# Optimization experiments

Hardware: AMD Instinct MI355X
Metric: run time of the kernel (lower is better)

Reference implementation:

```python
import jax, jax.numpy as jnp
import numpy as np

N_NODES = 50000
N_EDGES = 800000
IN_C, HID_C, OUT_C = 128, 128, 64


def setup_inputs() -> dict:
    key = jax.random.key(0)
    ks = jax.random.split(key, 12)
    glorot = lambda k, shape: jax.random.normal(k, shape, dtype=jnp.float32) * (2.0 / (shape[0] + shape[-1])) ** 0.5
    return {
        "x": jax.random.normal(ks[0], (N_NODES, IN_C), dtype=jnp.float32),
        "edge_index": jax.random.randint(ks[1], (2, N_EDGES), 0, N_NODES, dtype=jnp.int64),
        "W_s1": glorot(ks[2], (IN_C, HID_C)), "b_s1": jnp.zeros((HID_C,), jnp.float32),
        "W_s2": glorot(ks[3], (HID_C, HID_C)), "b_s2": jnp.zeros((HID_C,), jnp.float32),
        "W_m1": glorot(ks[4], (IN_C, HID_C)), "b_m1": jnp.zeros((HID_C,), jnp.float32),
        "W_m21": glorot(ks[5], (IN_C, HID_C)), "b_m21": jnp.zeros((HID_C,), jnp.float32),
        "W_m22": glorot(ks[6], (HID_C, HID_C)), "b_m22": jnp.zeros((HID_C,), jnp.float32),
        "W_att": glorot(ks[7], (HID_C, 1)), "b_att": jnp.zeros((1,), jnp.float32),
        "W_fc": glorot(ks[8], (2 * HID_C, OUT_C)), "b_fc": jnp.zeros((OUT_C,), jnp.float32),
    }


def _gcn_conv(x, W, b, src, dst, n_nodes):
    """PyG GCNConv: add self-loops, symmetric deg^-1/2 norm, linear, scatter-add, bias."""
    xw = x @ W  # [N, H]
    loop = jnp.arange(n_nodes, dtype=src.dtype)
    s = jnp.concatenate([src, loop])
    d = jnp.concatenate([dst, loop])
    ones = jnp.ones(s.shape[0], dtype=x.dtype)
    deg = jax.ops.segment_sum(ones, d, num_segments=n_nodes)  # in-degree incl. self loop
    dinv = jnp.where(deg > 0, jax.lax.rsqrt(deg), 0.0)
    norm = dinv[s] * dinv[d]  # [E+N]
    msg = xw[s] * norm[:, None]
    return jax.ops.segment_sum(msg, d, num_segments=n_nodes) + b


def reference(x, edge_index, W_s1, b_s1, W_s2, b_s2, W_m1, b_m1, W_m21, b_m21,
              W_m22, b_m22, W_att, b_att, W_fc, b_fc):
    n = x.shape[0]
    src, dst = edge_index[0], edge_index[1]
    # structural branch: two GCN layers
    h_struct = jax.nn.relu(_gcn_conv(x, W_s1, b_s1, src, dst, n))
    h_struct = jax.nn.relu(_gcn_conv(h_struct, W_s2, b_s2, src, dst, n))
    # meta branches
    h1 = jax.nn.relu(_gcn_conv(x, W_m1, b_m1, src, dst, n))
    h2 = jax.nn.relu(_gcn_conv(x, W_m21, b_m21, src, dst, n))
    h2 = jax.nn.relu(_gcn_conv(h2, W_m22, b_m22, src, dst, n))
    # attention-weighted fusion over the 2 branches
    H = jnp.stack([h1, h2], axis=1)  # [N, 2, H]
    attn_scores = H @ W_att + b_att  # [N, 2, 1]
    attn_weights = jax.nn.softmax(attn_scores, axis=1)
    h_meta = jnp.sum(attn_weights * H, axis=1)  # [N, H]
    h_comb = jnp.concatenate([h_struct, h_meta], axis=1)  # [N, 2H]
    return h_comb @ W_fc + b_fc  # [N, OUT_C]
```

## Files before the change

### kernel.cpp

```cpp
#include <hip/hip_runtime.h>
#include <hip/hip_bf16.h>

#define N_NODES 50000
#define N_EDGES 800000
#define IN_C 128
#define HID_C 128
#define OUT_C 64

#define SCAN_BS 256
#define SCAN_NB ((N_NODES + SCAN_BS - 1) / SCAN_BS)

typedef __attribute__((ext_vector_type(8))) short bf16x8;
typedef __attribute__((ext_vector_type(4))) float f32x4;

__device__ __forceinline__ ushort f2bf(float f) {
    unsigned u = __float_as_uint(f);
    return (ushort)((u + 0x7fffu + ((u >> 16) & 1u)) >> 16);
}
__device__ __forceinline__ float bf2f(ushort u) {
    return __uint_as_float(((unsigned)u) << 16);
}

__global__ void degree_kernel(const int* __restrict__ dst, int E, int* __restrict__ hist) {
    int e = blockIdx.x * blockDim.x + threadIdx.x;
    if (e < E) atomicAdd(&hist[dst[e]], 1);
}

__global__ void dinv_kernel(const int* __restrict__ hist, float* __restrict__ dinv, int n) {
    int i = blockIdx.x * blockDim.x + threadIdx.x;
    if (i < n) dinv[i] = rsqrtf((float)(hist[i] + 1));
}

__global__ __launch_bounds__(SCAN_BS)
void scan1_kernel(const int* __restrict__ hist, int* __restrict__ bsum, int n) {
    __shared__ int s[SCAN_BS];
    int t = threadIdx.x;
    int i = blockIdx.x * SCAN_BS + t;
    int v = (i < n) ? hist[i] : 0;
    s[t] = v;
    __syncthreads();
#pragma unroll
    for (int off = SCAN_BS / 2; off > 0; off >>= 1) {
        if (t < off) s[t] += s[t + off];
        __syncthreads();
    }
    if (t == 0) bsum[blockIdx.x] = s[0];
}

__global__ __launch_bounds__(SCAN_BS)
void scan2_kernel(int* __restrict__ bsum, int* __restrict__ bpre, int nb,
                  int* __restrict__ row_ptr_last, int n) {
    __shared__ int s[SCAN_BS];
    int t = threadIdx.x;
    int v = (t < nb) ? bsum[t] : 0;
    s[t] = v;
    __syncthreads();
#pragma unroll
    for (int off = 1; off < SCAN_BS; off <<= 1) {
        int tmp = (t >= off) ? s[t - off] : 0;
        __syncthreads();
        s[t] += tmp;
        __syncthreads();
    }
    if (t < nb) bpre[t] = s[t] - v;
    if (t == SCAN_BS - 1) row_ptr_last[n] = s[t];
}

__global__ __launch_bounds__(SCAN_BS)
void scan3_kernel(const int* __restrict__ hist, const int* __restrict__ bpre,
                  int* __restrict__ row_ptr, int* __restrict__ cursor, int n) {
    __shared__ int s[SCAN_BS];
    int t = threadIdx.x;
    int i = blockIdx.x * SCAN_BS + t;
    int v = (i < n) ? hist[i] : 0;
    s[t] = v;
    __syncthreads();
#pragma unroll
    for (int off = 1; off < SCAN_BS; off <<= 1) {
        int tmp = (t >= off) ? s[t - off] : 0;
        __syncthreads();
        s[t] += tmp;
        __syncthreads();
    }
    if (i < n) {
        int ex = s[t] - v + bpre[blockIdx.x];
        row_ptr[i] = ex;
        cursor[i]  = ex;
    }
}

__global__ void fill_kernel(const int* __restrict__ src, const int* __restrict__ dst, int E,
                            int* __restrict__ cursor, int2* __restrict__ edge_data,
                            const float* __restrict__ dinv) {
    int e = blockIdx.x * blockDim.x + threadIdx.x;
    if (e < E) {
        int d = dst[e];
        int s = src[e];
        int pos = atomicAdd(&cursor[d], 1);
        edge_data[pos] = make_int2(s, __float_as_int(dinv[s]));
    }
}

__global__ void cvt_bf16_kernel(const float* __restrict__ in, uint2* __restrict__ out, int n4) {
    int i = blockIdx.x * blockDim.x + threadIdx.x;
    if (i >= n4) return;
    float4 v = *(const float4*)&in[(size_t)i * 4];
    uint2 o;
    o.x = (uint)f2bf(v.x) | ((uint)f2bf(v.y) << 16);
    o.y = (uint)f2bf(v.z) | ((uint)f2bf(v.w) << 16);
    out[i] = o;
}

__global__ void pack_wcat_kernel(const float* __restrict__ Ws1, const float* __restrict__ Wm21,
                                 const float* __restrict__ Wm1,
                                 const float* __restrict__ bs1, const float* __restrict__ bm21,
                                 const float* __restrict__ bm1,
                                 ushort* __restrict__ Wt, float* __restrict__ bcat) {
    int idx = blockIdx.x * blockDim.x + threadIdx.x;
    if (idx < 384 * 128) {
        int c = idx >> 7, k = idx & 127;
        float v = (c < 128) ? Ws1[k * 128 + c]
                : (c < 256) ? Wm21[k * 128 + (c - 128)]
                            : Wm1[k * 128 + (c - 256)];
        Wt[idx] = f2bf(v);
    }
    if (idx < 384) {
        bcat[idx] = (idx < 128) ? bs1[idx] : (idx < 256) ? bm21[idx - 128] : bm1[idx - 256];
    }
}

__global__ void tpack_kernel(const float* __restrict__ W, ushort* __restrict__ Wt, int K, int C) {
    int idx = blockIdx.x * blockDim.x + threadIdx.x;
    if (idx >= K * C) return;
    int c = idx / K, k = idx % K;
    Wt[idx] = f2bf(W[(size_t)k * C + c]);
}

template<int C>
__global__ __launch_bounds__(256)
void agg_bf16(const ushort* __restrict__ X, int ldx,
              ushort* __restrict__ Y, int ldy,
              const int* __restrict__ row_ptr,
              const int2* __restrict__ edge_data,
              const float* __restrict__ dinv, int n) {
    constexpr int CG = C / 8;
    constexpr int SLOTS = 64 / CG;
    const int wid = blockIdx.x * (blockDim.x >> 6) + (threadIdx.x >> 6);
    if (wid >= n) return;
    const int lane = threadIdx.x & 63;
    const int cg = lane & (CG - 1);
    const int slot = lane / CG;

    const float di = dinv[wid];
    float acc[8] = {0.f, 0.f, 0.f, 0.f, 0.f, 0.f, 0.f, 0.f};

    auto fma_row = [&](uint4 v, float w) {
        acc[0] = fmaf(w, __uint_as_float(v.x << 16), acc[0]);
        acc[1] = fmaf(w, __uint_as_float(v.x & 0xffff0000u), acc[1]);
        acc[2] = fmaf(w, __uint_as_float(v.y << 16), acc[2]);
        acc[3] = fmaf(w, __uint_as_float(v.y & 0xffff0000u), acc[3]);
        acc[4] = fmaf(w, __uint_as_float(v.z << 16), acc[4]);
        acc[5] = fmaf(w, __uint_as_float(v.z & 0xffff0000u), acc[5]);
        acc[6] = fmaf(w, __uint_as_float(v.w << 16), acc[6]);
        acc[7] = fmaf(w, __uint_as_float(v.w & 0xffff0000u), acc[7]);
    };

    if (slot == 0) {
        uint4 v = *(const uint4*)&X[(size_t)wid * ldx + cg * 8];
        fma_row(v, di * di);
    }
    const int e0 = row_ptr[wid], e1 = row_ptr[wid + 1];
    int e = e0 + slot;
    for (; e + SLOTS < e1; e += 2 * SLOTS) {
        const int2 d0 = edge_data[e];
        const int2 d1 = edge_data[e + SLOTS];
        const uint4 v0 = *(const uint4*)&X[(size_t)d0.x * ldx + cg * 8];
        const uint4 v1 = *(const uint4*)&X[(size_t)d1.x * ldx + cg * 8];
        fma_row(v0, di * __int_as_float(d0.y));
        fma_row(v1, di * __int_as_float(d1.y));
    }
    if (e < e1) {
        const int2 d0 = edge_data[e];
        const uint4 v0 = *(const uint4*)&X[(size_t)d0.x * ldx + cg * 8];
        fma_row(v0, di * __int_as_float(d0.y));
    }
#pragma unroll
    for (int j = 0; j < 8; ++j) {
        if (SLOTS == 4) acc[j] += __shfl_xor(acc[j], 16);
        if (SLOTS >= 2) acc[j] += __shfl_xor(acc[j], 32);
    }
    if (slot == 0) {
        uint4 o;
        o.x = (uint)f2bf(acc[0]) | ((uint)f2bf(acc[1]) << 16);
        o.y = (uint)f2bf(acc[2]) | ((uint)f2bf(acc[3]) << 16);
        o.z = (uint)f2bf(acc[4]) | ((uint)f2bf(acc[5]) << 16);
        o.w = (uint)f2bf(acc[6]) | ((uint)f2bf(acc[7]) << 16);
        *(uint4*)&Y[(size_t)wid * ldy + cg * 8] = o;
    }
}

__global__ __launch_bounds__(256)
void mfma_gemm_kernel(const ushort* __restrict__ A, int lda,
                      const ushort* __restrict__ Wt,
                      const float* __restrict__ bias,
                      void* __restrict__ Yv, int ldy,
                      int M, int relu, int obf16) {
    __shared__ char Asmem[128 * 272];
    const int tid = threadIdx.x;
    const int lane = tid & 63;
    const int w = tid >> 6;
    const int rb = blockIdx.x * 128;
    const int cb = blockIdx.y * 128;

    {
        const int rowbase = tid >> 4;
        const int inrow = (tid & 15) * 8;
#pragma unroll
        for (int it = 0; it < 8; ++it) {
            int row = it * 16 + rowbase;
            uint4 v = make_uint4(0u, 0u, 0u, 0u);
            int r = rb + row;
            if (r < M) v = *(const uint4*)&A[(size_t)r * lda + inrow];
            *(uint4*)&Asmem[row * 272 + (tid & 15) * 16] = v;
        }
    }
    __syncthreads();

    f32x4 acc[2][8];
#pragma unroll
    for (int i = 0; i < 2; ++i)
#pragma unroll
        for (int j = 0; j < 8; ++j) acc[i][j] = (f32x4){0.f, 0.f, 0.f, 0.f};

    const int arow0 = w * 32 + (lane & 15);
    const int kq = (lane >> 4) * 8;
    const int ccol = lane & 15;
#pragma unroll
    for (int ks = 0; ks < 4; ++ks) {
        const int k0 = ks * 32;
        const bf16x8 a0 = *(const bf16x8*)&Asmem[arow0 * 272 + (k0 + kq) * 2];
        const bf16x8 a1 = *(const bf16x8*)&Asmem[(arow0 + 16) * 272 + (k0 + kq) * 2];
#pragma unroll
        for (int ct = 0; ct < 8; ++ct) {
            const bf16x8 b = *(const bf16x8*)&Wt[(size_t)(cb + ct * 16 + ccol) * 128 + k0 + kq];
            acc[0][ct] = __builtin_amdgcn_mfma_f32_16x16x32_bf16(a0, b, acc[0][ct], 0, 0, 0);
            acc[1][ct] = __builtin_amdgcn_mfma_f32_16x16x32_bf16(a1, b, acc[1][ct], 0, 0, 0);
        }
    }

    const int rowq = (lane >> 4) * 4;
#pragma unroll
    for (int rt = 0; rt < 2; ++rt) {
#pragma unroll
        for (int ct = 0; ct < 8; ++ct) {
            const int col = cb + ct * 16 + ccol;
            const float bcol = bias[col];
#pragma unroll
            for (int r = 0; r < 4; ++r) {
                const int row = rb + w * 32 + rt * 16 + rowq + r;
                if (row >= M) continue;
                float v = acc[rt][ct][r] + bcol;
                if (relu) v = fmaxf(v, 0.f);
                if (obf16) ((ushort*)Yv)[(size_t)row * ldy + col] = f2bf(v);
                else       ((float*)Yv)[(size_t)row * ldy + col] = v;
            }
        }
    }
}

__global__ __launch_bounds__(256)
void gemm_kernel(const float* __restrict__ X, int ldx,
                 const float* __restrict__ W, int ldw,
                 const float* __restrict__ bias,
                 void* __restrict__ Yv, int ldy,
                 int nrows, int K, int relu, int obf16) {
    __shared__ float Xs[64][68];
    __shared__ float Ws[64][68];
    const int tid = threadIdx.x;
    const int tx = tid & 15;
    const int ty = tid >> 4;
    const int rb = blockIdx.x * 64;
    const int cb = blockIdx.y * 64;

    float acc[4][4] = {{0.f}};

    for (int k0 = 0; k0 < K; k0 += 64) {
#pragma unroll
        for (int q = 0; q < 4; ++q) {
            int idx = tid + q * 256;
            int row = idx >> 4;
            int kq  = idx & 15;
            float4 v = make_float4(0.f, 0.f, 0.f, 0.f);
            int r = rb + row;
            if (r < nrows) v = *(const float4*)&X[(size_t)r * ldx + k0 + kq * 4];
            Xs[kq * 4 + 0][row] = v.x;
            Xs[kq * 4 + 1][row] = v.y;
            Xs[kq * 4 + 2][row] = v.z;
            Xs[kq * 4 + 3][row] = v.w;
        }
#pragma unroll
        for (int q = 0; q < 4; ++q) {
            int idx = tid + q * 256;
            int k  = idx >> 4;
            int c4 = idx & 15;
            float4 v = *(const float4*)&W[(size_t)(k0 + k) * ldw + cb + c4 * 4];
            *(float4*)&Ws[k][c4 * 4] = v;
        }
        __syncthreads();
#pragma unroll 16
        for (int k = 0; k < 64; ++k) {
            const float4 xv = *(const float4*)&Xs[k][ty * 4];
            const float4 wv = *(const float4*)&Ws[k][tx * 4];
            const float xr[4] = {xv.x, xv.y, xv.z, xv.w};
            const float wr[4] = {wv.x, wv.y, wv.z, wv.w};
#pragma unroll
            for (int i = 0; i < 4; ++i)
#pragma unroll
                for (int j = 0; j < 4; ++j)
                    acc[i][j] = fmaf(xr[i], wr[j], acc[i][j]);
        }
        __syncthreads();
    }

    const float4 bv = *(const float4*)&bias[cb + tx * 4];
    const float br[4] = {bv.x, bv.y, bv.z, bv.w};
#pragma unroll
    for (int i = 0; i < 4; ++i) {
        int r = rb + ty * 4 + i;
        if (r >= nrows) continue;
        float v0 = acc[i][0] + br[0];
        float v1 = acc[i][1] + br[1];
        float v2 = acc[i][2] + br[2];
        float v3 = acc[i][3] + br[3];
        if (relu) {
            v0 = fmaxf(v0, 0.f); v1 = fmaxf(v1, 0.f);
            v2 = fmaxf(v2, 0.f); v3 = fmaxf(v3, 0.f);
        }
        if (obf16) {
            ushort4 o;
            o.x = f2bf(v0); o.y = f2bf(v1); o.z = f2bf(v2); o.w = f2bf(v3);
            *(ushort4*)&((ushort*)Yv)[(size_t)r * ldy + cb + tx * 4] = o;
        } else {
            *(float4*)&((float*)Yv)[(size_t)r * ldy + cb + tx * 4] = make_float4(v0, v1, v2, v3);
        }
    }
}

__global__ __launch_bounds__(64)
void attn_kernel(const ushort* __restrict__ h1bf, const float* __restrict__ h2,
                 const float* __restrict__ Watt, const float* __restrict__ batt,
                 float* __restrict__ out, int ldout) {
    int i = blockIdx.x;
    int l = threadIdx.x;
    const ushort* h1p = &h1bf[(size_t)i * 384 + 256];
    float w0 = Watt[l], w1w = Watt[l + 64];
    float h1a = bf2f(h1p[l]),               h1b = bf2f(h1p[l + 64]);
    float h2a = h2[(size_t)i * 128 + l],    h2b = h2[(size_t)i * 128 + l + 64];
    float a = h1a * w0 + h1b * w1w;
    float b = h2a * w0 + h2b * w1w;
#pragma unroll
    for (int off = 32; off > 0; off >>= 1) {
        a += __shfl_xor(a, off);
        b += __shfl_xor(b, off);
    }
    float ba = batt[0];
    a += ba; b += ba;
    float m  = fmaxf(a, b);
    float ea = __expf(a - m), eb = __expf(b - m);
    float inv = 1.f / (ea + eb);
    float wa = ea * inv, wb = eb * inv;
    out[(size_t)i * ldout + l]      = wa * h1a + wb * h2a;
    out[(size_t)i * ldout + l + 64] = wa * h1b + wb * h2b;
}

extern "C" void kernel_launch(void* const* d_in, const int* in_sizes, int n_in,
                              void* d_out, int out_size, void* d_ws, size_t ws_size,
                              hipStream_t stream) {
    const int N = N_NODES, E = N_EDGES;
    const float* x     = (const float*)d_in[0];
    const int*   ei    = (const int*)d_in[1];
    const int*   esrc  = ei;
    const int*   edst  = ei + E;
    const float* W_s1  = (const float*)d_in[2];
    const float* b_s1  = (const float*)d_in[3];
    const float* W_s2  = (const float*)d_in[4];
    const float* b_s2  = (const float*)d_in[5];
    const float* W_m1  = (const float*)d_in[6];
    const float* b_m1  = (const float*)d_in[7];
    const float* W_m21 = (const float*)d_in[8];
    const float* b_m21 = (const float*)d_in[9];
    const float* W_m22 = (const float*)d_in[10];
    const float* b_m22 = (const float*)d_in[11];
    const float* W_att = (const float*)d_in[12];
    const float* b_att = (const float*)d_in[13];
    const float* W_fc  = (const float*)d_in[14];
    const float* b_fc  = (const float*)d_in[15];
    float* out = (float*)d_out;

    char* base = (char*)d_ws;
    size_t off = 0;
    auto take = [&](size_t nbytes) -> void* {
        void* p = base + off;
        off += (nbytes + 255) & ~(size_t)255;
        return p;
    };
    int*    hist      = (int*)take((size_t)N * 4);
    int*    cursor    = (int*)take((size_t)N * 4);
    int*    row_ptr   = (int*)take((size_t)(N + 1) * 4);
    int*    bsum      = (int*)take((size_t)SCAN_NB * 4);
    int*    bpre      = (int*)take((size_t)SCAN_NB * 4);
    int2*   edge_data = (int2*)take((size_t)E * 8);
    float*  dinv      = (float*)take((size_t)N * 4);
    ushort* xb        = (ushort*)take((size_t)N * 128 * 2);
    ushort* agg_x     = (ushort*)take((size_t)N * 128 * 2);
    ushort* cat1      = (ushort*)take((size_t)N * 384 * 2);
    ushort* bufB      = (ushort*)take((size_t)N * 256 * 2);
    float*  comb      = (float*)take((size_t)N * 256 * 4);
    float*  h2buf     = (float*)take((size_t)N * 128 * 4);
    ushort* Wcat_t    = (ushort*)take((size_t)384 * 128 * 2);
    ushort* Ws2_t     = (ushort*)take((size_t)128 * 128 * 2);
    ushort* Wm22_t    = (ushort*)take((size_t)128 * 128 * 2);
    float*  bcat      = (float*)take((size_t)384 * 4);

    hipMemsetAsync(hist, 0, (size_t)N * 4, stream);
    degree_kernel<<<(E + 255) / 256, 256, 0, stream>>>(edst, E, hist);
    dinv_kernel<<<(N + 255) / 256, 256, 0, stream>>>(hist, dinv, N);
    scan1_kernel<<<SCAN_NB, SCAN_BS, 0, stream>>>(hist, bsum, N);
    scan2_kernel<<<1, SCAN_BS, 0, stream>>>(bsum, bpre, SCAN_NB, row_ptr, N);
    scan3_kernel<<<SCAN_NB, SCAN_BS, 0, stream>>>(hist, bpre, row_ptr, cursor, N);
    fill_kernel<<<(E + 255) / 256, 256, 0, stream>>>(esrc, edst, E, cursor, edge_data, dinv);

    cvt_bf16_kernel<<<(N * 128 / 4 + 255) / 256, 256, 0, stream>>>(x, (uint2*)xb, N * 128 / 4);
    pack_wcat_kernel<<<(384 * 128 + 255) / 256, 256, 0, stream>>>(W_s1, W_m21, W_m1,
                                                                  b_s1, b_m21, b_m1, Wcat_t, bcat);
    tpack_kernel<<<(128 * 128 + 255) / 256, 256, 0, stream>>>(W_s2, Ws2_t, 128, 128);
    tpack_kernel<<<(128 * 128 + 255) / 256, 256, 0, stream>>>(W_m22, Wm22_t, 128, 128);

    agg_bf16<128><<<(N + 3) / 4, 256, 0, stream>>>(xb, 128, agg_x, 128, row_ptr, edge_data, dinv, N);

    dim3 gm384((N + 127) / 128, 3);
    dim3 gm128((N + 127) / 128, 1);
    mfma_gemm_kernel<<<gm384, 256, 0, stream>>>(agg_x, 128, Wcat_t, bcat, cat1, 384, N, 1, 1);

    agg_bf16<256><<<(N + 3) / 4, 256, 0, stream>>>(cat1, 384, bufB, 256, row_ptr, edge_data, dinv, N);

    mfma_gemm_kernel<<<gm128, 256, 0, stream>>>(bufB, 256, Ws2_t, b_s2, comb, 256, N, 1, 0);
    mfma_gemm_kernel<<<gm128, 256, 0, stream>>>(bufB + 128, 256, Wm22_t, b_m22, h2buf, 128, N, 1, 0);

    attn_kernel<<<N, 64, 0, stream>>>(cat1, h2buf, W_att, b_att, comb + 128, 256);

    dim3 g64((N + 63) / 64, 1);
    gemm_kernel<<<g64, 256, 0, stream>>>(comb, 256, W_fc, 64, b_fc, out, 64, N, 256, 0, 0);
}
```

Before: 423.7 us.

## Replace FP32 final FC GEMM with bf16 MFMA kernel and store intermediates as bf16

The scalar FP32 tiled GEMM for the final fully connected layer is replaced with a bf16 MFMA kernel that stages a 64-row A tile in shared memory and reads transposed bf16 weights. The struct and meta-branch GEMM outputs and the attention output are now stored as bf16 rather than fp32, which halves their memory traffic. The aggregation loop is also unrolled to four edges per slot so more gathers are in flight. The cost is extra bf16 rounding on intermediate activations and one more weight-transpose launch.

After: 414.0 us. -2.3%, faster.

```diff
diff --git a/kernel.cpp b/kernel.cpp
--- a/kernel.cpp
+++ b/kernel.cpp
@@ -171,15 +171,21 @@
     }
     const int e0 = row_ptr[wid], e1 = row_ptr[wid + 1];
     int e = e0 + slot;
-    for (; e + SLOTS < e1; e += 2 * SLOTS) {
+    for (; e + 3 * SLOTS < e1; e += 4 * SLOTS) {
         const int2 d0 = edge_data[e];
         const int2 d1 = edge_data[e + SLOTS];
+        const int2 d2 = edge_data[e + 2 * SLOTS];
+        const int2 d3 = edge_data[e + 3 * SLOTS];
         const uint4 v0 = *(const uint4*)&X[(size_t)d0.x * ldx + cg * 8];
         const uint4 v1 = *(const uint4*)&X[(size_t)d1.x * ldx + cg * 8];
+        const uint4 v2 = *(const uint4*)&X[(size_t)d2.x * ldx + cg * 8];
+        const uint4 v3 = *(const uint4*)&X[(size_t)d3.x * ldx + cg * 8];
         fma_row(v0, di * __int_as_float(d0.y));
         fma_row(v1, di * __int_as_float(d1.y));
-    }
-    if (e < e1) {
+        fma_row(v2, di * __int_as_float(d2.y));
+        fma_row(v3, di * __int_as_float(d3.y));
+    }
+    for (; e < e1; e += SLOTS) {
         const int2 d0 = edge_data[e];
         const uint4 v0 = *(const uint4*)&X[(size_t)d0.x * ldx + cg * 8];
         fma_row(v0, di * __int_as_float(d0.y));
@@ -269,93 +275,72 @@
 }
 
 __global__ __launch_bounds__(256)
-void gemm_kernel(const float* __restrict__ X, int ldx,
-                 const float* __restrict__ W, int ldw,
-                 const float* __restrict__ bias,
-                 void* __restrict__ Yv, int ldy,
-                 int nrows, int K, int relu, int obf16) {
-    __shared__ float Xs[64][68];
-    __shared__ float Ws[64][68];
+void mfma_fc_kernel(const ushort* __restrict__ A,
+                    const ushort* __restrict__ Wt,
+                    const float* __restrict__ bias,
+                    float* __restrict__ Y, int M) {
+    __shared__ char Asmem[64 * 528];
     const int tid = threadIdx.x;
-    const int tx = tid & 15;
-    const int ty = tid >> 4;
+    const int lane = tid & 63;
+    const int w = tid >> 6;
     const int rb = blockIdx.x * 64;
-    const int cb = blockIdx.y * 64;
-
-    float acc[4][4] = {{0.f}};
-
-    for (int k0 = 0; k0 < K; k0 += 64) {
-#pragma unroll
-        for (int q = 0; q < 4; ++q) {
-            int idx = tid + q * 256;
-            int row = idx >> 4;
-            int kq  = idx & 15;
-            float4 v = make_float4(0.f, 0.f, 0.f, 0.f);
+
+    {
+        const int rowbase = tid >> 5;
+        const int seg = (tid & 31);
+#pragma unroll
+        for (int it = 0; it < 8; ++it) {
+            int row = it * 8 + rowbase;
+            uint4 v = make_uint4(0u, 0u, 0u, 0u);
             int r = rb + row;
-            if (r < nrows) v = *(const float4*)&X[(size_t)r * ldx + k0 + kq * 4];
-            Xs[kq * 4 + 0][row] = v.x;
-            Xs[kq * 4 + 1][row] = v.y;
-            Xs[kq * 4 + 2][row] = v.z;
-            Xs[kq * 4 + 3][row] = v.w;
-        }
-#pragma unroll
-        for (int q = 0; q < 4; ++q) {
-            int idx = tid + q * 256;
-            int k  = idx >> 4;
-            int c4 = idx & 15;
-            float4 v = *(const float4*)&W[(size_t)(k0 + k) * ldw + cb + c4 * 4];
-            *(float4*)&Ws[k][c4 * 4] = v;
-        }
-        __syncthreads();
-#pragma unroll 16
-        for (int k = 0; k < 64; ++k) {
-            const float4 xv = *(const float4*)&Xs[k][ty * 4];
-            const float4 wv = *(const float4*)&Ws[k][tx * 4];
-            const float xr[4] = {xv.x, xv.y, xv.z, xv.w};
-            const float wr[4] = {wv.x, wv.y, wv.z, wv.w};
-#pragma unroll
-            for (int i = 0; i < 4; ++i)
-#pragma unroll
-                for (int j = 0; j < 4; ++j)
-                    acc[i][j] = fmaf(xr[i], wr[j], acc[i][j]);
-        }
-        __syncthreads();
-    }
-
-    const float4 bv = *(const float4*)&bias[cb + tx * 4];
-    const float br[4] = {bv.x, bv.y, bv.z, bv.w};
-#pragma unroll
-    for (int i = 0; i < 4; ++i) {
-        int r = rb + ty * 4 + i;
-        if (r >= nrows) continue;
-        float v0 = acc[i][0] + br[0];
-        float v1 = acc[i][1] + br[1];
-        float v2 = acc[i][2] + br[2];
-        float v3 = acc[i][3] + br[3];
-        if (relu) {
-            v0 = fmaxf(v0, 0.f); v1 = fmaxf(v1, 0.f);
-            v2 = fmaxf(v2, 0.f); v3 = fmaxf(v3, 0.f);
-        }
-        if (obf16) {
-            ushort4 o;
-            o.x = f2bf(v0); o.y = f2bf(v1); o.z = f2bf(v2); o.w = f2bf(v3);
-            *(ushort4*)&((ushort*)Yv)[(size_t)r * ldy + cb + tx * 4] = o;
-        } else {
-            *(float4*)&((float*)Yv)[(size_t)r * ldy + cb + tx * 4] = make_float4(v0, v1, v2, v3);
+            if (r < M) v = *(const uint4*)&A[(size_t)r * 256 + seg * 8];
+            *(uint4*)&Asmem[row * 528 + seg * 16] = v;
+        }
+    }
+    __syncthreads();
+
+    f32x4 acc[4];
+#pragma unroll
+    for (int j = 0; j < 4; ++j) acc[j] = (f32x4){0.f, 0.f, 0.f, 0.f};
+
+    const int arow = w * 16 + (lane & 15);
+    const int kq = (lane >> 4) * 8;
+    const int ccol = lane & 15;
+#pragma unroll
+    for (int ks = 0; ks < 8; ++ks) {
+        const int k0 = ks * 32;
+        const bf16x8 a = *(const bf16x8*)&Asmem[arow * 528 + (k0 + kq) * 2];
+#pragma unroll
+        for (int ct = 0; ct < 4; ++ct) {
+            const bf16x8 b = *(const bf16x8*)&Wt[(size_t)(ct * 16 + ccol) * 256 + k0 + kq];
+            acc[ct] = __builtin_amdgcn_mfma_f32_16x16x32_bf16(a, b, acc[ct], 0, 0, 0);
+        }
+    }
+
+    const int rowq = (lane >> 4) * 4;
+#pragma unroll
+    for (int ct = 0; ct < 4; ++ct) {
+        const int col = ct * 16 + ccol;
+        const float bcol = bias[col];
+#pragma unroll
+        for (int r = 0; r < 4; ++r) {
+            const int row = rb + w * 16 + rowq + r;
+            if (row < M) Y[(size_t)row * 64 + col] = acc[ct][r] + bcol;
         }
     }
 }
 
 __global__ __launch_bounds__(64)
-void attn_kernel(const ushort* __restrict__ h1bf, const float* __restrict__ h2,
+void attn_kernel(const ushort* __restrict__ h1bf, const ushort* __restrict__ h2bf,
                  const float* __restrict__ Watt, const float* __restrict__ batt,
-                 float* __restrict__ out, int ldout) {
+                 ushort* __restrict__ outb, int ldout) {
     int i = blockIdx.x;
     int l = threadIdx.x;
     const ushort* h1p = &h1bf[(size_t)i * 384 + 256];
+    const ushort* h2p = &h2bf[(size_t)i * 128];
     float w0 = Watt[l], w1w = Watt[l + 64];
-    float h1a = bf2f(h1p[l]),               h1b = bf2f(h1p[l + 64]);
-    float h2a = h2[(size_t)i * 128 + l],    h2b = h2[(size_t)i * 128 + l + 64];
+    float h1a = bf2f(h1p[l]), h1b = bf2f(h1p[l + 64]);
+    float h2a = bf2f(h2p[l]), h2b = bf2f(h2p[l + 64]);
     float a = h1a * w0 + h1b * w1w;
     float b = h2a * w0 + h2b * w1w;
 #pragma unroll
@@ -369,8 +354,8 @@
     float ea = __expf(a - m), eb = __expf(b - m);
     float inv = 1.f / (ea + eb);
     float wa = ea * inv, wb = eb * inv;
-    out[(size_t)i * ldout + l]      = wa * h1a + wb * h2a;
-    out[(size_t)i * ldout + l + 64] = wa * h1b + wb * h2b;
+    outb[(size_t)i * ldout + l]      = f2bf(wa * h1a + wb * h2a);
+    outb[(size_t)i * ldout + l + 64] = f2bf(wa * h1b + wb * h2b);
 }
 
 extern "C" void kernel_launch(void* const* d_in, const int* in_sizes, int n_in,
@@ -415,11 +400,12 @@
     ushort* agg_x     = (ushort*)take((size_t)N * 128 * 2);
     ushort* cat1      = (ushort*)take((size_t)N * 384 * 2);
     ushort* bufB      = (ushort*)take((size_t)N * 256 * 2);
-    float*  comb      = (float*)take((size_t)N * 256 * 4);
-    float*  h2buf     = (float*)take((size_t)N * 128 * 4);
+    ushort* comb      = (ushort*)take((size_t)N * 256 * 2);
+    ushort* h2buf     = (ushort*)take((size_t)N * 128 * 2);
     ushort* Wcat_t    = (ushort*)take((size_t)384 * 128 * 2);
     ushort* Ws2_t     = (ushort*)take((size_t)128 * 128 * 2);
     ushort* Wm22_t    = (ushort*)take((size_t)128 * 128 * 2);
+    ushort* Wfc_t     = (ushort*)take((size_t)64 * 256 * 2);
     float*  bcat      = (float*)take((size_t)384 * 4);
 
     hipMemsetAsync(hist, 0, (size_t)N * 4, stream);
@@ -435,6 +421,7 @@
                                                                   b_s1, b_m21, b_m1, Wcat_t, bcat);
     tpack_kernel<<<(128 * 128 + 255) / 256, 256, 0, stream>>>(W_s2, Ws2_t, 128, 128);
     tpack_kernel<<<(128 * 128 + 255) / 256, 256, 0, stream>>>(W_m22, Wm22_t, 128, 128);
+    tpack_kernel<<<(256 * 64 + 255) / 256, 256, 0, stream>>>(W_fc, Wfc_t, 256, 64);
 
     agg_bf16<128><<<(N + 3) / 4, 256, 0, stream>>>(xb, 128, agg_x, 128, row_ptr, edge_data, dinv, N);
 
@@ -444,11 +431,10 @@
 
     agg_bf16<256><<<(N + 3) / 4, 256, 0, stream>>>(cat1, 384, bufB, 256, row_ptr, edge_data, dinv, N);
 
-    mfma_gemm_kernel<<<gm128, 256, 0, stream>>>(bufB, 256, Ws2_t, b_s2, comb, 256, N, 1, 0);
-    mfma_gemm_kernel<<<gm128, 256, 0, stream>>>(bufB + 128, 256, Wm22_t, b_m22, h2buf, 128, N, 1, 0);
+    mfma_gemm_kernel<<<gm128, 256, 0, stream>>>(bufB, 256, Ws2_t, b_s2, comb, 256, N, 1, 1);
+    mfma_gemm_kernel<<<gm128, 256, 0, stream>>>(bufB + 128, 256, Wm22_t, b_m22, h2buf, 128, N, 1, 1);
 
     attn_kernel<<<N, 64, 0, stream>>>(cat1, h2buf, W_att, b_att, comb + 128, 256);
 
-    dim3 g64((N + 63) / 64, 1);
-    gemm_kernel<<<g64, 256, 0, stream>>>(comb, 256, W_fc, 64, b_fc, out, 64, N, 256, 0, 0);
-}
+    mfma_fc_kernel<<<(N + 63) / 64, 256, 0, stream>>>(comb, Wfc_t, b_fc, out, N);
+}
```
